# Performance work log

Hardware: AMD Instinct MI355X
Metric: run time of the kernel (lower is better)

## Reference

```python
import jax, jax.numpy as jnp
import numpy as np

N_VIEWS = 8


def _trilinear(vol, pts):
    """Trilinear interpolation of vol [Nx,Ny,Nz] at pts [...,3] (voxel coords), zero outside."""
    nx, ny, nz = vol.shape
    x, y, z = pts[..., 0], pts[..., 1], pts[..., 2]
    x0f, y0f, z0f = jnp.floor(x), jnp.floor(y), jnp.floor(z)
    fx, fy, fz = x - x0f, y - y0f, z - z0f
    x0 = x0f.astype(jnp.int32)
    y0 = y0f.astype(jnp.int32)
    z0 = z0f.astype(jnp.int32)
    out = jnp.zeros(x.shape, vol.dtype)
    for dx in (0, 1):
        wx = fx if dx else (1.0 - fx)
        ix = x0 + dx
        vx = (ix >= 0) & (ix < nx)
        ixc = jnp.clip(ix, 0, nx - 1)
        for dy in (0, 1):
            wy = fy if dy else (1.0 - fy)
            iy = y0 + dy
            vxy = vx & (iy >= 0) & (iy < ny)
            iyc = jnp.clip(iy, 0, ny - 1)
            for dz in (0, 1):
                wz = fz if dz else (1.0 - fz)
                iz = z0 + dz
                valid = vxy & (iz >= 0) & (iz < nz)
                izc = jnp.clip(iz, 0, nz - 1)
                v = vol[ixc, iyc, izc]  # irregular gather
                out = out + jnp.where(valid, v, jnp.zeros((), vol.dtype)) * (wx * wy * wz)
    return out


def cone_project(vol, src_pos, det_center, det_u_vec, det_v_vec,
                 det_u, det_v, du, dv, voxel_spacing, n_steps):
    """Cone-beam forward projection: ray-march src->detector pixel, trilinear sampling."""
    nx, ny, nz = vol.shape
    us = (jnp.arange(det_u, dtype=vol.dtype) - (det_u - 1) / 2.0) * du
    vs = (jnp.arange(det_v, dtype=vol.dtype) - (det_v - 1) / 2.0) * dv
    # detector pixel world positions: [V, U, W, 3]
    det_pts = (det_center[:, None, None, :]
               + us[None, :, None, None] * det_u_vec[:, None, None, :]
               + vs[None, None, :, None] * det_v_vec[:, None, None, :])
    src = src_pos[:, None, None, :]            # [V,1,1,3]
    diff = det_pts - src                        # [V,U,W,3]
    ray_len = jnp.sqrt(jnp.sum(diff * diff, axis=-1))  # [V,U,W]
    step_len = ray_len / n_steps
    center = (jnp.array([nx, ny, nz], dtype=vol.dtype) - 1.0) / 2.0
    fracs = (jnp.arange(n_steps, dtype=vol.dtype) + 0.5) / n_steps

    def body(acc, s):
        p = src + s * diff                      # world coords [V,U,W,3]
        vox = p / voxel_spacing + center        # voxel coords
        return acc + _trilinear(vol, vox), None

    acc, _ = jax.lax.scan(body, jnp.zeros(ray_len.shape, vol.dtype), fracs)
    return acc * step_len


def setup_inputs() -> dict:
    key = jax.random.key(0)
    k1, k2 = jax.random.split(key)
    vol_shape = (256, 256, 256)
    x = 0.1 * jax.random.normal(k1, vol_shape, dtype=jnp.float32)
    reco = 0.1 * jax.random.normal(k2, vol_shape, dtype=jnp.float32)
    # circular cone-beam trajectory (units = voxels, spacing 1.0)
    sad, sdd = 400.0, 800.0  # source-axis / source-detector distance
    angles = np.linspace(0.0, np.pi, N_VIEWS, endpoint=False)
    ca, sa = np.cos(angles), np.sin(angles)
    zeros = np.zeros(N_VIEWS)
    src_pos = np.stack([-sad * ca, -sad * sa, zeros], axis=-1)
    det_center = np.stack([(sdd - sad) * ca, (sdd - sad) * sa, zeros], axis=-1)
    det_u_vec = np.stack([-sa, ca, zeros], axis=-1)
    det_v_vec = np.tile(np.array([0.0, 0.0, 1.0]), (N_VIEWS, 1))
    return {
        "x": x,
        "reco": reco,
        "src_pos": jnp.asarray(src_pos, jnp.float32),
        "det_center": jnp.asarray(det_center, jnp.float32),
        "det_u_vec": jnp.asarray(det_u_vec, jnp.float32),
        "det_v_vec": jnp.asarray(det_v_vec, jnp.float32),
        "du": 3.0,
        "dv": 3.0,
        "voxel_spacing": 1.0,
        "det_u": 128,
        "det_v": 128,
        "n_steps": 192,
    }


def reference(x, reco, src_pos, det_center, det_u_vec, det_v_vec,
              du, dv, voxel_spacing, det_u, det_v, n_steps):
    updated = x + reco
    sino = cone_project(updated, src_pos, det_center, det_u_vec, det_v_vec,
                        det_u, det_v, du, dv, voxel_spacing, n_steps)
    return sino, jax.nn.relu(updated)
```

## Files before the change

kernel.cpp:

```cpp
#include <hip/hip_runtime.h>
#include <math.h>

typedef float nfloat4 __attribute__((ext_vector_type(4)));

__global__ __launch_bounds__(256) void add_relu_kernel(
    const float* __restrict__ x,
    const float* __restrict__ reco,
    float* __restrict__ relu_out,
    float* __restrict__ upd_out,
    int n4)
{
    int i = blockIdx.x * blockDim.x + threadIdx.x;
    int stride = gridDim.x * blockDim.x;
    const nfloat4* x4 = (const nfloat4*)x;
    const nfloat4* r4 = (const nfloat4*)reco;
    nfloat4* ro4 = (nfloat4*)relu_out;
    nfloat4* uo4 = (nfloat4*)upd_out;
    for (; i < n4; i += stride) {
        nfloat4 a = x4[i];
        nfloat4 b = r4[i];
        nfloat4 u = a + b;
        if (uo4) uo4[i] = u;
        nfloat4 r;
        r.x = fmaxf(u.x, 0.f); r.y = fmaxf(u.y, 0.f);
        r.z = fmaxf(u.z, 0.f); r.w = fmaxf(u.w, 0.f);
        ro4[i] = r;
    }
}

__device__ __forceinline__ void clip_axis(float a, float b, float lo, float hi,
                                          float& t_lo, float& t_hi)
{
    if (fabsf(b) > 1e-6f) {
        float t0 = (lo - a) / b;
        float t1 = (hi - a) / b;
        float tmn = fminf(t0, t1);
        float tmx = fmaxf(t0, t1);
        t_lo = fmaxf(t_lo, tmn);
        t_hi = fminf(t_hi, tmx);
    } else {
        if (a <= lo || a >= hi) { t_lo = 1.0f; t_hi = 0.0f; }
    }
}

template <int TWO>
__device__ __forceinline__ float sample_step(
    const float* __restrict__ vol_a,
    const float* __restrict__ vol_b,
    float s,
    float sx, float sy, float sz,
    float dx, float dy, float dz,
    float inv_sp, float cx, float cy, float cz,
    int nx, int ny, int nz, bool live_step)
{
    const float px = fmaf(s, dx, sx) * inv_sp + cx;
    const float py = fmaf(s, dy, sy) * inv_sp + cy;
    const float pz = fmaf(s, dz, sz) * inv_sp + cz;

    const float x0f = floorf(px);
    const float y0f = floorf(py);
    const float z0f = floorf(pz);
    const float fx = px - x0f;
    const float fy = py - y0f;
    const float fz = pz - z0f;
    const int x0 = (int)x0f;
    const int y0 = (int)y0f;
    const int z0 = (int)z0f;

    const bool vx0 = (unsigned)x0 < (unsigned)nx;
    const bool vx1 = (unsigned)(x0 + 1) < (unsigned)nx;
    const bool vy0 = (unsigned)y0 < (unsigned)ny;
    const bool vy1 = (unsigned)(y0 + 1) < (unsigned)ny;
    const bool vz0 = live_step & ((unsigned)z0 < (unsigned)nz);
    const bool vz1 = live_step & ((unsigned)(z0 + 1) < (unsigned)nz);

    const int xc0 = min(max(x0, 0), nx - 1);
    const int xc1 = min(max(x0 + 1, 0), nx - 1);
    const int yc0 = min(max(y0, 0), ny - 1);
    const int yc1 = min(max(y0 + 1, 0), ny - 1);
    const int zc0 = min(max(z0, 0), nz - 1);
    const int zc1 = min(max(z0 + 1, 0), nz - 1);

    const int r00 = (xc0 * ny + yc0) * nz;
    const int r01 = (xc0 * ny + yc1) * nz;
    const int r10 = (xc1 * ny + yc0) * nz;
    const int r11 = (xc1 * ny + yc1) * nz;

    float v000 = vol_a[r00 + zc0];
    float v001 = vol_a[r00 + zc1];
    float v010 = vol_a[r01 + zc0];
    float v011 = vol_a[r01 + zc1];
    float v100 = vol_a[r10 + zc0];
    float v101 = vol_a[r10 + zc1];
    float v110 = vol_a[r11 + zc0];
    float v111 = vol_a[r11 + zc1];
    if (TWO) {
        v000 += vol_b[r00 + zc0];
        v001 += vol_b[r00 + zc1];
        v010 += vol_b[r01 + zc0];
        v011 += vol_b[r01 + zc1];
        v100 += vol_b[r10 + zc0];
        v101 += vol_b[r10 + zc1];
        v110 += vol_b[r11 + zc0];
        v111 += vol_b[r11 + zc1];
    }

    const float gx = 1.0f - fx;
    const float gy = 1.0f - fy;
    const float gz = 1.0f - fz;
    const float wxy00 = gx * gy;
    const float wxy01 = gx * fy;
    const float wxy10 = fx * gy;
    const float wxy11 = fx * fy;

    const float w000 = (vx0 & vy0 & vz0) ? wxy00 * gz : 0.0f;
    const float w001 = (vx0 & vy0 & vz1) ? wxy00 * fz : 0.0f;
    const float w010 = (vx0 & vy1 & vz0) ? wxy01 * gz : 0.0f;
    const float w011 = (vx0 & vy1 & vz1) ? wxy01 * fz : 0.0f;
    const float w100 = (vx1 & vy0 & vz0) ? wxy10 * gz : 0.0f;
    const float w101 = (vx1 & vy0 & vz1) ? wxy10 * fz : 0.0f;
    const float w110 = (vx1 & vy1 & vz0) ? wxy11 * gz : 0.0f;
    const float w111 = (vx1 & vy1 & vz1) ? wxy11 * fz : 0.0f;

    float samp = 0.0f;
    samp = fmaf(w000, v000, samp);
    samp = fmaf(w001, v001, samp);
    samp = fmaf(w010, v010, samp);
    samp = fmaf(w011, v011, samp);
    samp = fmaf(w100, v100, samp);
    samp = fmaf(w101, v101, samp);
    samp = fmaf(w110, v110, samp);
    samp = fmaf(w111, v111, samp);
    return samp;
}

template <int TWO>
__global__ __launch_bounds__(256, 4) void cone_project_seg_kernel(
    const float* __restrict__ vol_a,
    const float* __restrict__ vol_b,
    const float* __restrict__ src_pos,
    const float* __restrict__ det_center,
    const float* __restrict__ det_u_vec,
    const float* __restrict__ det_v_vec,
    const float* __restrict__ du_p,
    const float* __restrict__ dv_p,
    const float* __restrict__ spacing_p,
    const int* __restrict__ det_u_p,
    const int* __restrict__ det_v_p,
    const int* __restrict__ nsteps_p,
    float* __restrict__ sino,
    int n_views, int nx, int ny, int nz)
{
    const int det_u = *det_u_p;
    const int det_v = *det_v_p;
    const int n_steps = *nsteps_p;
    const float du = *du_p;
    const float dv = *dv_p;
    const float inv_sp = 1.0f / *spacing_p;

    const long total = (long)n_views * det_u * det_v;
    const int pix = threadIdx.x & 63;
    const int seg = threadIdx.x >> 6;

    int bid = blockIdx.x;
    if ((gridDim.x & 7) == 0) {
        const int cpx = (int)(gridDim.x >> 3);
        bid = (bid & 7) * cpx + (bid >> 3);
    }

    const long idx = (long)bid * 64 + pix;
    const bool live = idx < total;

    const long cidx = live ? idx : 0;
    const int v = (int)(cidx % det_v);
    const int u = (int)((cidx / det_v) % det_u);
    const int view = (int)(cidx / ((long)det_u * det_v));

    const float us = ((float)u - (det_u - 1) * 0.5f) * du;
    const float vs = ((float)v - (det_v - 1) * 0.5f) * dv;

    const float sx = src_pos[view * 3 + 0];
    const float sy = src_pos[view * 3 + 1];
    const float sz = src_pos[view * 3 + 2];

    const float dpx = det_center[view * 3 + 0] + us * det_u_vec[view * 3 + 0] + vs * det_v_vec[view * 3 + 0];
    const float dpy = det_center[view * 3 + 1] + us * det_u_vec[view * 3 + 1] + vs * det_v_vec[view * 3 + 1];
    const float dpz = det_center[view * 3 + 2] + us * det_u_vec[view * 3 + 2] + vs * det_v_vec[view * 3 + 2];

    const float dx = dpx - sx;
    const float dy = dpy - sy;
    const float dz = dpz - sz;
    const float ray_len = sqrtf(dx * dx + dy * dy + dz * dz);
    const float step_len = ray_len / (float)n_steps;

    const float cx = (nx - 1) * 0.5f;
    const float cy = (ny - 1) * 0.5f;
    const float cz = (nz - 1) * 0.5f;

    float t_lo = 0.0f, t_hi = 1.0f;
    clip_axis(sx * inv_sp + cx, dx * inv_sp, -1.0f, (float)nx, t_lo, t_hi);
    clip_axis(sy * inv_sp + cy, dy * inv_sp, -1.0f, (float)ny, t_lo, t_hi);
    clip_axis(sz * inv_sp + cz, dz * inv_sp, -1.0f, (float)nz, t_lo, t_hi);

    int i_min = 0, i_max = -1;
    if (t_hi > t_lo) {
        i_min = (int)floorf(t_lo * (float)n_steps - 0.5f) - 1;
        i_max = (int)ceilf(t_hi * (float)n_steps - 0.5f) + 1;
        i_min = max(i_min, 0);
        i_max = min(i_max, n_steps - 1);
    }
    if (!live) { i_min = 0; i_max = -1; }

    const int count = i_max - i_min + 1;
    const int per8 = (count + 7) >> 3;
    const int isA = i_min + seg * per8;
    const int isB = i_min + (seg + 4) * per8;
    const int ieA = min(isA + per8 - 1, i_max);
    const int ieB = min(isB + per8 - 1, i_max);

    const float inv_n = 1.0f / (float)n_steps;

    float accA = 0.0f;
    float accB = 0.0f;
    for (int j = 0; j < per8; ++j) {
        const int iA = isA + j;
        const int iB = isB + j;
        const float sA = ((float)iA + 0.5f) * inv_n;
        const float sB = ((float)iB + 0.5f) * inv_n;
        accA += sample_step<TWO>(vol_a, vol_b, sA, sx, sy, sz, dx, dy, dz,
                                 inv_sp, cx, cy, cz, nx, ny, nz, iA <= ieA);
        accB += sample_step<TWO>(vol_a, vol_b, sB, sx, sy, sz, dx, dy, dz,
                                 inv_sp, cx, cy, cz, nx, ny, nz, iB <= ieB);
    }
    const float acc = accA + accB;

    __shared__ float red[256];
    red[threadIdx.x] = acc;
    __syncthreads();
    if (seg == 0 && live) {
        float tot = red[pix] + red[pix + 64] + red[pix + 128] + red[pix + 192];
        sino[idx] = tot * step_len;
    }
}

extern "C" void kernel_launch(void* const* d_in, const int* in_sizes, int n_in,
                              void* d_out, int out_size, void* d_ws, size_t ws_size,
                              hipStream_t stream) {
    const float* x          = (const float*)d_in[0];
    const float* reco       = (const float*)d_in[1];
    const float* src_pos    = (const float*)d_in[2];
    const float* det_center = (const float*)d_in[3];
    const float* det_u_vec  = (const float*)d_in[4];
    const float* det_v_vec  = (const float*)d_in[5];
    const float* du_p       = (const float*)d_in[6];
    const float* dv_p       = (const float*)d_in[7];
    const float* spacing_p  = (const float*)d_in[8];
    const int*   det_u_p    = (const int*)d_in[9];
    const int*   det_v_p    = (const int*)d_in[10];
    const int*   nsteps_p   = (const int*)d_in[11];

    const int n_vol = in_sizes[0];
    const int n_views = in_sizes[2] / 3;

    int n = 1;
    while ((long)(n + 1) * (n + 1) * (n + 1) <= (long)n_vol) ++n;
    const int nx = n, ny = n, nz = n;

    const int sino_size = out_size - n_vol;
    float* sino     = (float*)d_out;
    float* relu_out = (float*)d_out + sino_size;

    const bool use_ws = ws_size >= (size_t)n_vol * sizeof(float);
    float* upd = (float*)d_ws;

    const int n4 = n_vol / 4;
    add_relu_kernel<<<2048, 256, 0, stream>>>(
        x, reco, relu_out, use_ws ? upd : nullptr, n4);

    const int blocks = (sino_size + 63) / 64;
    if (use_ws) {
        cone_project_seg_kernel<0><<<blocks, 256, 0, stream>>>(
            upd, nullptr,
            src_pos, det_center, det_u_vec, det_v_vec,
            du_p, dv_p, spacing_p, det_u_p, det_v_p, nsteps_p,
            sino, n_views, nx, ny, nz);
    } else {
        cone_project_seg_kernel<1><<<blocks, 256, 0, stream>>>(
            x, reco,
            src_pos, det_center, det_u_vec, det_v_vec,
            du_p, dv_p, spacing_p, det_u_p, det_v_p, nsteps_p,
            sino, n_views, nx, ny, nz);
    }
}
```

Before: 237.4 us.

## Fuse add-relu and cone projection into one interleaved launch, gather from both inputs

Merges the elementwise add+relu kernel and the ray-marching projection into one kernel whose even blocks march rays and odd blocks do the add+relu. The updated volume is no longer written to workspace; each trilinear tap instead gathers from both x and reco and adds them. It also drops the XCD-aware block index remapping. This removes one launch and the workspace write/read, at the cost of doubling gather traffic per sample and possibly worse L2 locality across chiplets.

```diff
diff --git a/kernel.cpp b/kernel.cpp
--- a/kernel.cpp
+++ b/kernel.cpp
@@ -2,31 +2,6 @@
 #include <math.h>
 
 typedef float nfloat4 __attribute__((ext_vector_type(4)));
-
-__global__ __launch_bounds__(256) void add_relu_kernel(
-    const float* __restrict__ x,
-    const float* __restrict__ reco,
-    float* __restrict__ relu_out,
-    float* __restrict__ upd_out,
-    int n4)
-{
-    int i = blockIdx.x * blockDim.x + threadIdx.x;
-    int stride = gridDim.x * blockDim.x;
-    const nfloat4* x4 = (const nfloat4*)x;
-    const nfloat4* r4 = (const nfloat4*)reco;
-    nfloat4* ro4 = (nfloat4*)relu_out;
-    nfloat4* uo4 = (nfloat4*)upd_out;
-    for (; i < n4; i += stride) {
-        nfloat4 a = x4[i];
-        nfloat4 b = r4[i];
-        nfloat4 u = a + b;
-        if (uo4) uo4[i] = u;
-        nfloat4 r;
-        r.x = fmaxf(u.x, 0.f); r.y = fmaxf(u.y, 0.f);
-        r.z = fmaxf(u.z, 0.f); r.w = fmaxf(u.w, 0.f);
-        ro4[i] = r;
-    }
-}
 
 __device__ __forceinline__ void clip_axis(float a, float b, float lo, float hi,
                                           float& t_lo, float& t_hi)
@@ -43,7 +18,6 @@
     }
 }
 
-template <int TWO>
 __device__ __forceinline__ float sample_step(
     const float* __restrict__ vol_a,
     const float* __restrict__ vol_b,
@@ -86,24 +60,14 @@
     const int r10 = (xc1 * ny + yc0) * nz;
     const int r11 = (xc1 * ny + yc1) * nz;
 
-    float v000 = vol_a[r00 + zc0];
-    float v001 = vol_a[r00 + zc1];
-    float v010 = vol_a[r01 + zc0];
-    float v011 = vol_a[r01 + zc1];
-    float v100 = vol_a[r10 + zc0];
-    float v101 = vol_a[r10 + zc1];
-    float v110 = vol_a[r11 + zc0];
-    float v111 = vol_a[r11 + zc1];
-    if (TWO) {
-        v000 += vol_b[r00 + zc0];
-        v001 += vol_b[r00 + zc1];
-        v010 += vol_b[r01 + zc0];
-        v011 += vol_b[r01 + zc1];
-        v100 += vol_b[r10 + zc0];
-        v101 += vol_b[r10 + zc1];
-        v110 += vol_b[r11 + zc0];
-        v111 += vol_b[r11 + zc1];
-    }
+    float v000 = vol_a[r00 + zc0] + vol_b[r00 + zc0];
+    float v001 = vol_a[r00 + zc1] + vol_b[r00 + zc1];
+    float v010 = vol_a[r01 + zc0] + vol_b[r01 + zc0];
+    float v011 = vol_a[r01 + zc1] + vol_b[r01 + zc1];
+    float v100 = vol_a[r10 + zc0] + vol_b[r10 + zc0];
+    float v101 = vol_a[r10 + zc1] + vol_b[r10 + zc1];
+    float v110 = vol_a[r11 + zc0] + vol_b[r11 + zc0];
+    float v111 = vol_a[r11 + zc1] + vol_b[r11 + zc1];
 
     const float gx = 1.0f - fx;
     const float gy = 1.0f - fy;
@@ -134,10 +98,9 @@
     return samp;
 }
 
-template <int TWO>
-__global__ __launch_bounds__(256, 4) void cone_project_seg_kernel(
-    const float* __restrict__ vol_a,
-    const float* __restrict__ vol_b,
+__global__ __launch_bounds__(256, 4) void fused_kernel(
+    const float* __restrict__ x,
+    const float* __restrict__ reco,
     const float* __restrict__ src_pos,
     const float* __restrict__ det_center,
     const float* __restrict__ det_u_vec,
@@ -149,8 +112,31 @@
     const int* __restrict__ det_v_p,
     const int* __restrict__ nsteps_p,
     float* __restrict__ sino,
-    int n_views, int nx, int ny, int nz)
+    float* __restrict__ relu_out,
+    int n_views, int nx, int ny, int nz, int n4)
 {
+    const bool is_cone = (blockIdx.x & 1) == 0;
+    const int sub = blockIdx.x >> 1;
+    const int half_blocks = gridDim.x >> 1;
+
+    if (!is_cone) {
+        int i = sub * blockDim.x + threadIdx.x;
+        const int stride = half_blocks * blockDim.x;
+        const nfloat4* x4 = (const nfloat4*)x;
+        const nfloat4* r4 = (const nfloat4*)reco;
+        nfloat4* ro4 = (nfloat4*)relu_out;
+        for (; i < n4; i += stride) {
+            nfloat4 a = x4[i];
+            nfloat4 b = r4[i];
+            nfloat4 u = a + b;
+            nfloat4 r;
+            r.x = fmaxf(u.x, 0.f); r.y = fmaxf(u.y, 0.f);
+            r.z = fmaxf(u.z, 0.f); r.w = fmaxf(u.w, 0.f);
+            ro4[i] = r;
+        }
+        return;
+    }
+
     const int det_u = *det_u_p;
     const int det_v = *det_v_p;
     const int n_steps = *nsteps_p;
@@ -162,13 +148,7 @@
     const int pix = threadIdx.x & 63;
     const int seg = threadIdx.x >> 6;
 
-    int bid = blockIdx.x;
-    if ((gridDim.x & 7) == 0) {
-        const int cpx = (int)(gridDim.x >> 3);
-        bid = (bid & 7) * cpx + (bid >> 3);
-    }
-
-    const long idx = (long)bid * 64 + pix;
+    const long idx = (long)sub * 64 + pix;
     const bool live = idx < total;
 
     const long cidx = live ? idx : 0;
@@ -227,10 +207,10 @@
         const int iB = isB + j;
         const float sA = ((float)iA + 0.5f) * inv_n;
         const float sB = ((float)iB + 0.5f) * inv_n;
-        accA += sample_step<TWO>(vol_a, vol_b, sA, sx, sy, sz, dx, dy, dz,
-                                 inv_sp, cx, cy, cz, nx, ny, nz, iA <= ieA);
-        accB += sample_step<TWO>(vol_a, vol_b, sB, sx, sy, sz, dx, dy, dz,
-                                 inv_sp, cx, cy, cz, nx, ny, nz, iB <= ieB);
+        accA += sample_step(x, reco, sA, sx, sy, sz, dx, dy, dz,
+                            inv_sp, cx, cy, cz, nx, ny, nz, iA <= ieA);
+        accB += sample_step(x, reco, sB, sx, sy, sz, dx, dy, dz,
+                            inv_sp, cx, cy, cz, nx, ny, nz, iB <= ieB);
     }
     const float acc = accA + accB;
 
@@ -270,25 +250,14 @@
     float* sino     = (float*)d_out;
     float* relu_out = (float*)d_out + sino_size;
 
-    const bool use_ws = ws_size >= (size_t)n_vol * sizeof(float);
-    float* upd = (float*)d_ws;
-
     const int n4 = n_vol / 4;
-    add_relu_kernel<<<2048, 256, 0, stream>>>(
-        x, reco, relu_out, use_ws ? upd : nullptr, n4);
-
-    const int blocks = (sino_size + 63) / 64;
-    if (use_ws) {
-        cone_project_seg_kernel<0><<<blocks, 256, 0, stream>>>(
-            upd, nullptr,
-            src_pos, det_center, det_u_vec, det_v_vec,
-            du_p, dv_p, spacing_p, det_u_p, det_v_p, nsteps_p,
-            sino, n_views, nx, ny, nz);
-    } else {
-        cone_project_seg_kernel<1><<<blocks, 256, 0, stream>>>(
-            x, reco,
-            src_pos, det_center, det_u_vec, det_v_vec,
-            du_p, dv_p, spacing_p, det_u_p, det_v_p, nsteps_p,
-            sino, n_views, nx, ny, nz);
-    }
-}
+    const int cone_blocks = (sino_size + 63) / 64;
+    const int grid = 2 * cone_blocks;
+
+    fused_kernel<<<grid, 256, 0, stream>>>(
+        x, reco,
+        src_pos, det_center, det_u_vec, det_v_vec,
+        du_p, dv_p, spacing_p, det_u_p, det_v_p, nsteps_p,
+        sino, relu_out,
+        n_views, nx, ny, nz, n4);
+}
```

Result: slower. 296.5 us (+24.9%).

## Add wave-uniform ray-marching path exploiting shared x/y coordinates across detector rows

Applied to the files above, without the earlier changes.

Adds a specialized sampling path used when the detector v-axis is purely along z and det_v is a multiple of 64. In that case all 64 lanes of a wavefront share view and u, so the x/y voxel indices at each step are identical across lanes. These indices are made scalar with readfirstlane, and the per-ray step range is widened to the wave-wide min/max via shuffles so every lane iterates the same steps. This is meant to reduce vector address arithmetic and divergence and to make the gathers contiguous along z. The cost is extra masked samples for lanes whose own range is shorter, and the fallback path is kept for other geometries.

```diff
diff --git a/kernel.cpp b/kernel.cpp
--- a/kernel.cpp
+++ b/kernel.cpp
@@ -1,5 +1,6 @@
 #include <hip/hip_runtime.h>
 #include <math.h>
+#include <limits.h>
 
 typedef float nfloat4 __attribute__((ext_vector_type(4)));
 
@@ -104,6 +105,85 @@
         v110 += vol_b[r11 + zc0];
         v111 += vol_b[r11 + zc1];
     }
+
+    const float gx = 1.0f - fx;
+    const float gy = 1.0f - fy;
+    const float gz = 1.0f - fz;
+    const float wxy00 = gx * gy;
+    const float wxy01 = gx * fy;
+    const float wxy10 = fx * gy;
+    const float wxy11 = fx * fy;
+
+    const float w000 = (vx0 & vy0 & vz0) ? wxy00 * gz : 0.0f;
+    const float w001 = (vx0 & vy0 & vz1) ? wxy00 * fz : 0.0f;
+    const float w010 = (vx0 & vy1 & vz0) ? wxy01 * gz : 0.0f;
+    const float w011 = (vx0 & vy1 & vz1) ? wxy01 * fz : 0.0f;
+    const float w100 = (vx1 & vy0 & vz0) ? wxy10 * gz : 0.0f;
+    const float w101 = (vx1 & vy0 & vz1) ? wxy10 * fz : 0.0f;
+    const float w110 = (vx1 & vy1 & vz0) ? wxy11 * gz : 0.0f;
+    const float w111 = (vx1 & vy1 & vz1) ? wxy11 * fz : 0.0f;
+
+    float samp = 0.0f;
+    samp = fmaf(w000, v000, samp);
+    samp = fmaf(w001, v001, samp);
+    samp = fmaf(w010, v010, samp);
+    samp = fmaf(w011, v011, samp);
+    samp = fmaf(w100, v100, samp);
+    samp = fmaf(w101, v101, samp);
+    samp = fmaf(w110, v110, samp);
+    samp = fmaf(w111, v111, samp);
+    return samp;
+}
+
+__device__ __forceinline__ float sample_step_u(
+    const float* __restrict__ vol,
+    float s,
+    float sx, float sy, float sz,
+    float dx, float dy, float dz,
+    float inv_sp, float cx, float cy, float cz,
+    int nx, int ny, int nz, bool live_step)
+{
+    const float px = fmaf(s, dx, sx) * inv_sp + cx;
+    const float py = fmaf(s, dy, sy) * inv_sp + cy;
+    const float pz = fmaf(s, dz, sz) * inv_sp + cz;
+
+    const float x0f = floorf(px);
+    const float y0f = floorf(py);
+    const float z0f = floorf(pz);
+    const float fx = px - x0f;
+    const float fy = py - y0f;
+    const float fz = pz - z0f;
+    const int x0 = __builtin_amdgcn_readfirstlane((int)x0f);
+    const int y0 = __builtin_amdgcn_readfirstlane((int)y0f);
+    const int z0 = (int)z0f;
+
+    const bool vx0 = (unsigned)x0 < (unsigned)nx;
+    const bool vx1 = (unsigned)(x0 + 1) < (unsigned)nx;
+    const bool vy0 = (unsigned)y0 < (unsigned)ny;
+    const bool vy1 = (unsigned)(y0 + 1) < (unsigned)ny;
+    const bool vz0 = live_step & ((unsigned)z0 < (unsigned)nz);
+    const bool vz1 = live_step & ((unsigned)(z0 + 1) < (unsigned)nz);
+
+    const int xc0 = min(max(x0, 0), nx - 1);
+    const int xc1 = min(max(x0 + 1, 0), nx - 1);
+    const int yc0 = min(max(y0, 0), ny - 1);
+    const int yc1 = min(max(y0 + 1, 0), ny - 1);
+    const int zc0 = min(max(z0, 0), nz - 1);
+    const int zc1 = min(max(z0 + 1, 0), nz - 1);
+
+    const float* row00 = vol + (xc0 * ny + yc0) * nz;
+    const float* row01 = vol + (xc0 * ny + yc1) * nz;
+    const float* row10 = vol + (xc1 * ny + yc0) * nz;
+    const float* row11 = vol + (xc1 * ny + yc1) * nz;
+
+    const float v000 = row00[zc0];
+    const float v001 = row00[zc1];
+    const float v010 = row01[zc0];
+    const float v011 = row01[zc1];
+    const float v100 = row10[zc0];
+    const float v101 = row10[zc1];
+    const float v110 = row11[zc0];
+    const float v111 = row11[zc1];
 
     const float gx = 1.0f - fx;
     const float gy = 1.0f - fy;
@@ -183,9 +263,13 @@
     const float sy = src_pos[view * 3 + 1];
     const float sz = src_pos[view * 3 + 2];
 
-    const float dpx = det_center[view * 3 + 0] + us * det_u_vec[view * 3 + 0] + vs * det_v_vec[view * 3 + 0];
-    const float dpy = det_center[view * 3 + 1] + us * det_u_vec[view * 3 + 1] + vs * det_v_vec[view * 3 + 1];
-    const float dpz = det_center[view * 3 + 2] + us * det_u_vec[view * 3 + 2] + vs * det_v_vec[view * 3 + 2];
+    const float dvx = det_v_vec[view * 3 + 0];
+    const float dvy = det_v_vec[view * 3 + 1];
+    const float dvz = det_v_vec[view * 3 + 2];
+
+    const float dpx = det_center[view * 3 + 0] + us * det_u_vec[view * 3 + 0] + vs * dvx;
+    const float dpy = det_center[view * 3 + 1] + us * det_u_vec[view * 3 + 1] + vs * dvy;
+    const float dpz = det_center[view * 3 + 2] + us * det_u_vec[view * 3 + 2] + vs * dvz;
 
     const float dx = dpx - sx;
     const float dy = dpy - sy;
@@ -211,26 +295,57 @@
     }
     if (!live) { i_min = 0; i_max = -1; }
 
-    const int count = i_max - i_min + 1;
-    const int per8 = (count + 7) >> 3;
-    const int isA = i_min + seg * per8;
-    const int isB = i_min + (seg + 4) * per8;
-    const int ieA = min(isA + per8 - 1, i_max);
-    const int ieB = min(isB + per8 - 1, i_max);
-
     const float inv_n = 1.0f / (float)n_steps;
-
     float accA = 0.0f;
     float accB = 0.0f;
-    for (int j = 0; j < per8; ++j) {
-        const int iA = isA + j;
-        const int iB = isB + j;
-        const float sA = ((float)iA + 0.5f) * inv_n;
-        const float sB = ((float)iB + 0.5f) * inv_n;
-        accA += sample_step<TWO>(vol_a, vol_b, sA, sx, sy, sz, dx, dy, dz,
-                                 inv_sp, cx, cy, cz, nx, ny, nz, iA <= ieA);
-        accB += sample_step<TWO>(vol_a, vol_b, sB, sx, sy, sz, dx, dy, dz,
-                                 inv_sp, cx, cy, cz, nx, ny, nz, iB <= ieB);
+
+    const bool uniform_ok = !TWO && ((det_v & 63) == 0) &&
+                            (dvx == 0.0f) && (dvy == 0.0f);
+
+    if (uniform_ok) {
+        int lo = (i_max < i_min) ? INT_MAX : i_min;
+        int hi = (i_max < i_min) ? INT_MIN : i_max;
+        for (int m = 1; m < 64; m <<= 1) {
+            lo = min(lo, __shfl_xor(lo, m));
+            hi = max(hi, __shfl_xor(hi, m));
+        }
+        if (hi < lo) { lo = 0; hi = -1; }
+
+        const int count = hi - lo + 1;
+        const int per8 = (count + 7) >> 3;
+        const int isA = lo + seg * per8;
+        const int isB = lo + (seg + 4) * per8;
+        const int ieA = min(isA + per8 - 1, hi);
+        const int ieB = min(isB + per8 - 1, hi);
+
+        for (int j = 0; j < per8; ++j) {
+            const int iA = isA + j;
+            const int iB = isB + j;
+            const float sA = ((float)iA + 0.5f) * inv_n;
+            const float sB = ((float)iB + 0.5f) * inv_n;
+            accA += sample_step_u(vol_a, sA, sx, sy, sz, dx, dy, dz,
+                                  inv_sp, cx, cy, cz, nx, ny, nz, iA <= ieA);
+            accB += sample_step_u(vol_a, sB, sx, sy, sz, dx, dy, dz,
+                                  inv_sp, cx, cy, cz, nx, ny, nz, iB <= ieB);
+        }
+    } else {
+        const int count = i_max - i_min + 1;
+        const int per8 = (count + 7) >> 3;
+        const int isA = i_min + seg * per8;
+        const int isB = i_min + (seg + 4) * per8;
+        const int ieA = min(isA + per8 - 1, i_max);
+        const int ieB = min(isB + per8 - 1, i_max);
+
+        for (int j = 0; j < per8; ++j) {
+            const int iA = isA + j;
+            const int iB = isB + j;
+            const float sA = ((float)iA + 0.5f) * inv_n;
+            const float sB = ((float)iB + 0.5f) * inv_n;
+            accA += sample_step<TWO>(vol_a, vol_b, sA, sx, sy, sz, dx, dy, dz,
+                                     inv_sp, cx, cy, cz, nx, ny, nz, iA <= ieA);
+            accB += sample_step<TWO>(vol_a, vol_b, sB, sx, sy, sz, dx, dy, dz,
+                                     inv_sp, cx, cy, cz, nx, ny, nz, iB <= ieB);
+        }
     }
     const float acc = accA + accB;
 
```

Result: no change. 238.0 us (+0.3%).
